# Optimization experiments

Measured on AMD Instinct MI355X. Metric: run time of the kernel, lower is better.

The kernel has to match this reference:

```python
import jax, jax.numpy as jnp
import numpy as np

N = 500_000
MOL_C = 128
HID_C = 256
NUM_GRAPHS = 16384


def setup_inputs() -> dict:
    key = jax.random.key(0)
    ks = jax.random.split(key, 7)
    fan_lin = (MOL_C + HID_C) ** -0.5
    fan_last = HID_C ** -0.5
    return {
        "input_rep": jax.random.normal(ks[0], (N, MOL_C), dtype=jnp.float32),
        "final_rep": jax.random.normal(ks[1], (N, HID_C), dtype=jnp.float32),
        "graph_index": jnp.sort(jax.random.randint(ks[2], (N,), 0, NUM_GRAPHS, dtype=jnp.int32)),
        "W_lin": jax.random.normal(ks[3], (HID_C, MOL_C + HID_C), dtype=jnp.float32) * fan_lin,
        "b_lin": jax.random.normal(ks[4], (HID_C,), dtype=jnp.float32) * fan_lin,
        "W_last": jax.random.normal(ks[5], (HID_C, HID_C), dtype=jnp.float32) * fan_last,
        "b_last": jax.random.normal(ks[6], (HID_C,), dtype=jnp.float32) * fan_last,
    }


def reference(input_rep, final_rep, graph_index, W_lin, b_lin, W_last, b_last):
    # att = sigmoid(Linear(cat([input_rep, final_rep], dim=1)))  -> [N, HID_C]
    cat = jnp.concatenate([input_rep, final_rep], axis=1)
    att = jax.nn.sigmoid(cat @ W_lin.T + b_lin)
    # gated value: att * Linear(final_rep)  -> [N, HID_C]
    g = att * (final_rep @ W_last.T + b_last)
    # scatter_add over nodes -> [NUM_GRAPHS, HID_C]
    return jax.ops.segment_sum(g, graph_index, num_segments=NUM_GRAPHS)
```

## Files before the change

### kernel.cpp

```cpp
#include <hip/hip_runtime.h>
#include <hip/hip_bf16.h>

#define MOLC 128
#define HIDC 256
#define KTOT 384
#define TILE_N 128
#define NTHREADS 512
#define APAD 40
#define WPAD 40

typedef _Float16 f16;
typedef _Float16 f16x8 __attribute__((ext_vector_type(8)));
typedef float    f32x4 __attribute__((ext_vector_type(4)));

__device__ inline f16x8 cvt8(float4 a, float4 b) {
  f16x8 r;
  r[0] = (f16)a.x; r[1] = (f16)a.y; r[2] = (f16)a.z; r[3] = (f16)a.w;
  r[4] = (f16)b.x; r[5] = (f16)b.y; r[6] = (f16)b.z; r[7] = (f16)b.w;
  return r;
}

__global__ void zero_out_kernel(float4* __restrict__ p, int n4) {
  int i = blockIdx.x * blockDim.x + threadIdx.x;
  if (i < n4) p[i] = make_float4(0.f, 0.f, 0.f, 0.f);
}

__global__ __launch_bounds__(NTHREADS, 2) void attn_pool_kernel(
    const float* __restrict__ input_rep,
    const float* __restrict__ final_rep,
    const int*   __restrict__ gidx,
    const float* __restrict__ W_lin,
    const float* __restrict__ b_lin,
    const float* __restrict__ W_last,
    const float* __restrict__ b_last,
    float* __restrict__ out,
    int n_nodes)
{
  __shared__ f16 A_lds[TILE_N * APAD];
  __shared__ f16 W1_lds[HIDC * WPAD];
  __shared__ f16 W2_lds[HIDC * WPAD];
  __shared__ int gi_lds[TILE_N];

  const int t    = threadIdx.x;
  const int nb   = blockIdx.x * TILE_N;
  const int vn   = min(TILE_N, n_nodes - nb);

  const int lane = t & 63;
  const int w    = t >> 6;
  const int h    = w >> 2;
  const int wch  = (w & 3) * 64;
  const int lr   = lane & 15;
  const int lq   = lane >> 4;

  if (t < TILE_N) gi_lds[t] = (nb + t < n_nodes) ? gidx[nb + t] : -1;

  f32x4 acc1[4][4];
  f32x4 acc2[4][4];
#pragma unroll
  for (int i = 0; i < 4; ++i)
#pragma unroll
    for (int j = 0; j < 4; ++j) {
      acc1[i][j] = (f32x4)(0.f);
      acc2[i][j] = (f32x4)(0.f);
    }

  const int arow = t >> 2;
  const int acol = (t & 3) * 8;
  const int wrow = t >> 1;
  const int wcol = (t & 1) * 16;

  for (int ks = 0; ks < 12; ++ks) {
    const int k0 = ks * 32;

    {
      float4 x0, x1;
      if (arow < vn) {
        const float* src = (ks < 4)
            ? (input_rep + (size_t)(nb + arow) * MOLC + (k0 + acol))
            : (final_rep + (size_t)(nb + arow) * HIDC + (k0 - MOLC + acol));
        x0 = *(const float4*)src;
        x1 = *(const float4*)(src + 4);
      } else {
        x0 = make_float4(0.f, 0.f, 0.f, 0.f);
        x1 = x0;
      }
      *(f16x8*)&A_lds[arow * APAD + acol] = cvt8(x0, x1);
    }

    {
      const float* src = W_lin + (size_t)wrow * KTOT + (k0 + wcol);
      float4 a = ((const float4*)src)[0];
      float4 b = ((const float4*)src)[1];
      float4 c = ((const float4*)src)[2];
      float4 d = ((const float4*)src)[3];
      *(f16x8*)&W1_lds[wrow * WPAD + wcol]     = cvt8(a, b);
      *(f16x8*)&W1_lds[wrow * WPAD + wcol + 8] = cvt8(c, d);
    }

    if (ks >= 4) {
      const float* src = W_last + (size_t)wrow * HIDC + (k0 - MOLC + wcol);
      float4 a = ((const float4*)src)[0];
      float4 b = ((const float4*)src)[1];
      float4 c = ((const float4*)src)[2];
      float4 d = ((const float4*)src)[3];
      *(f16x8*)&W2_lds[wrow * WPAD + wcol]     = cvt8(a, b);
      *(f16x8*)&W2_lds[wrow * WPAD + wcol + 8] = cvt8(c, d);
    }

    __syncthreads();

    f16x8 af[4];
#pragma unroll
    for (int i = 0; i < 4; ++i)
      af[i] = *(const f16x8*)&A_lds[(h * 64 + i * 16 + lr) * APAD + lq * 8];

    {
      f16x8 bf[4];
#pragma unroll
      for (int j = 0; j < 4; ++j)
        bf[j] = *(const f16x8*)&W1_lds[(wch + j * 16 + lr) * WPAD + lq * 8];
#pragma unroll
      for (int i = 0; i < 4; ++i)
#pragma unroll
        for (int j = 0; j < 4; ++j)
          acc1[i][j] = __builtin_amdgcn_mfma_f32_16x16x32_f16(af[i], bf[j], acc1[i][j], 0, 0, 0);
    }
    if (ks >= 4) {
      f16x8 bf[4];
#pragma unroll
      for (int j = 0; j < 4; ++j)
        bf[j] = *(const f16x8*)&W2_lds[(wch + j * 16 + lr) * WPAD + lq * 8];
#pragma unroll
      for (int i = 0; i < 4; ++i)
#pragma unroll
        for (int j = 0; j < 4; ++j)
          acc2[i][j] = __builtin_amdgcn_mfma_f32_16x16x32_f16(af[i], bf[j], acc2[i][j], 0, 0, 0);
    }

    __syncthreads();
  }

  float bl[4], bb[4];
#pragma unroll
  for (int j = 0; j < 4; ++j) {
    bl[j] = b_lin[wch + j * 16 + lr];
    bb[j] = b_last[wch + j * 16 + lr];
  }
#pragma unroll
  for (int i = 0; i < 4; ++i)
#pragma unroll
    for (int j = 0; j < 4; ++j)
#pragma unroll
      for (int r = 0; r < 4; ++r) {
        float a   = acc1[i][j][r] + bl[j];
        float att = 1.f / (1.f + __expf(-a));
        acc1[i][j][r] = att * (acc2[i][j][r] + bb[j]);
      }

  for (int i = 0; i < 4; ++i) {
    const int base = h * 64 + i * 16;
    int myg[4];
#pragma unroll
    for (int r = 0; r < 4; ++r) myg[r] = gi_lds[base + lq * 4 + r];

    int s = 0;
    while (s < 16) {
      const int gid = gi_lds[base + s];
      int e = s + 1;
      while (e < 16 && gi_lds[base + e] == gid) ++e;
      if (gid >= 0) {
#pragma unroll
        for (int j = 0; j < 4; ++j) {
          float v = 0.f;
#pragma unroll
          for (int r = 0; r < 4; ++r)
            if (myg[r] == gid) v += acc1[i][j][r];
          v += __shfl_xor(v, 16);
          v += __shfl_xor(v, 32);
          if (lane < 16)
            atomicAdd(&out[(size_t)gid * HIDC + wch + j * 16 + lane], v);
        }
      }
      s = e;
    }
  }
}

extern "C" void kernel_launch(void* const* d_in, const int* in_sizes, int n_in,
                              void* d_out, int out_size, void* d_ws, size_t ws_size,
                              hipStream_t stream) {
  const float* input_rep = (const float*)d_in[0];
  const float* final_rep = (const float*)d_in[1];
  const int*   gidx      = (const int*)d_in[2];
  const float* W_lin     = (const float*)d_in[3];
  const float* b_lin     = (const float*)d_in[4];
  const float* W_last    = (const float*)d_in[5];
  const float* b_last    = (const float*)d_in[6];
  float* out = (float*)d_out;

  const int n_nodes = in_sizes[0] / MOLC;

  const int n4 = out_size / 4;
  zero_out_kernel<<<(n4 + 255) / 256, 256, 0, stream>>>((float4*)out, n4);

  const int grid = (n_nodes + TILE_N - 1) / TILE_N;
  attn_pool_kernel<<<grid, NTHREADS, 0, stream>>>(
      input_rep, final_rep, gidx, W_lin, b_lin, W_last, b_last, out, n_nodes);
}
```

Before: 1.242 ms.

## Prepack fp16 swizzled weights and double-buffer tiles with async LDS loads

Adds a pre-pass that converts W_lin and W_last to fp16 in a tile-major, XOR-swizzled layout in the workspace. The main kernel then stages weight tiles directly into LDS with global_load_lds and double-buffers weights and activations so the next K-slice loads overlap the MFMA work. The tile shrinks to 64 nodes with 256 threads, and the swizzle replaces LDS padding to avoid bank conflicts. This removes per-block fp32-to-fp16 weight conversion, but each block now re-reads the weights for half as many nodes, and one extra kernel launch is added.

```diff
diff --git a/kernel.cpp b/kernel.cpp
--- a/kernel.cpp
+++ b/kernel.cpp
@@ -1,124 +1,151 @@
 #include <hip/hip_runtime.h>
 #include <hip/hip_bf16.h>
+
 
 #define MOLC 128
 #define HIDC 256
 #define KTOT 384
-#define TILE_N 128
-#define NTHREADS 512
-#define APAD 40
-#define WPAD 40
+#define NKT  12
+#define TILE_N 64
+#define NTHREADS 256
 
 typedef _Float16 f16;
 typedef _Float16 f16x8 __attribute__((ext_vector_type(8)));
 typedef float    f32x4 __attribute__((ext_vector_type(4)));
 
-__device__ inline f16x8 cvt8(float4 a, float4 b) {
+__device__ __host__ __forceinline__ int swz(int r) { return (r ^ (r >> 2)) & 3; }
+
+__device__ __forceinline__ f16x8 cvt8(float4 a, float4 b) {
   f16x8 r;
   r[0] = (f16)a.x; r[1] = (f16)a.y; r[2] = (f16)a.z; r[3] = (f16)a.w;
   r[4] = (f16)b.x; r[5] = (f16)b.y; r[6] = (f16)b.z; r[7] = (f16)b.w;
   return r;
 }
 
+#define GLL16(g, l) __builtin_amdgcn_global_load_lds(                          \
+    (const __attribute__((address_space(1))) uint32_t*)(g),                    \
+    (__attribute__((address_space(3))) uint32_t*)(l), 16, 0, 0)
+
 __global__ void zero_out_kernel(float4* __restrict__ p, int n4) {
   int i = blockIdx.x * blockDim.x + threadIdx.x;
   if (i < n4) p[i] = make_float4(0.f, 0.f, 0.f, 0.f);
+}
+
+__global__ void pack_weights_kernel(const float* __restrict__ W_lin,
+                                    const float* __restrict__ W_last,
+                                    f16* __restrict__ ws) {
+  int s = blockIdx.x * blockDim.x + threadIdx.x;
+  if (s >= 20480) return;
+  const float* src;
+  f16* dst;
+  if (s < 12288) {
+    int ks = s >> 10, r = (s >> 2) & 255, c = s & 3;
+    src = W_lin + (size_t)r * KTOT + ks * 32 + ((c ^ swz(r)) * 8);
+    dst = ws + (size_t)s * 8;
+  } else {
+    int s2 = s - 12288;
+    int ks = s2 >> 10, r = (s2 >> 2) & 255, c = s2 & 3;
+    src = W_last + (size_t)r * HIDC + ks * 32 + ((c ^ swz(r)) * 8);
+    dst = ws + 98304 + (size_t)s2 * 8;
+  }
+  f16x8 v;
+#pragma unroll
+  for (int j = 0; j < 8; ++j) v[j] = (f16)src[j];
+  *(f16x8*)dst = v;
+}
+
+__device__ __forceinline__ void stage_w(const f16* gtile, f16* ltile, int wv, int lane) {
+#pragma unroll
+  for (int c = 0; c < 4; ++c) {
+    const int off = (wv * 4 + c) * 1024 + lane * 16;
+    GLL16((const char*)gtile + off, (char*)ltile + off);
+  }
 }
 
 __global__ __launch_bounds__(NTHREADS, 2) void attn_pool_kernel(
     const float* __restrict__ input_rep,
     const float* __restrict__ final_rep,
     const int*   __restrict__ gidx,
-    const float* __restrict__ W_lin,
+    const f16*   __restrict__ ws,
     const float* __restrict__ b_lin,
-    const float* __restrict__ W_last,
     const float* __restrict__ b_last,
     float* __restrict__ out,
     int n_nodes)
 {
-  __shared__ f16 A_lds[TILE_N * APAD];
-  __shared__ f16 W1_lds[HIDC * WPAD];
-  __shared__ f16 W2_lds[HIDC * WPAD];
-  __shared__ int gi_lds[TILE_N];
+  __shared__ f16 Abuf[2][TILE_N * 32];
+  __shared__ f16 W1buf[2][HIDC * 32];
+  __shared__ f16 W2buf[2][HIDC * 32];
+  __shared__ int gi[TILE_N];
 
   const int t    = threadIdx.x;
   const int nb   = blockIdx.x * TILE_N;
   const int vn   = min(TILE_N, n_nodes - nb);
-
   const int lane = t & 63;
-  const int w    = t >> 6;
-  const int h    = w >> 2;
-  const int wch  = (w & 3) * 64;
+  const int wv   = t >> 6;
+  const int wch  = wv * 64;
   const int lr   = lane & 15;
   const int lq   = lane >> 4;
-
-  if (t < TILE_N) gi_lds[t] = (nb + t < n_nodes) ? gidx[nb + t] : -1;
-
-  f32x4 acc1[4][4];
-  f32x4 acc2[4][4];
+  const int sl   = (lq ^ swz(lr)) * 8;
+
+  const int arow  = t >> 2;
+  const int aslot = t & 3;
+  const int awslot = (aslot ^ swz(arow)) * 8;
+
+  if (t < TILE_N) gi[t] = (nb + t < n_nodes) ? gidx[nb + t] : -1;
+
+  const f16* wsW1 = ws;
+  const f16* wsW2 = ws + 98304;
+
+  stage_w(wsW1, W1buf[0], wv, lane);
+  {
+    float4 x0, x1;
+    if (arow < vn) {
+      const float* src = input_rep + (size_t)(nb + arow) * MOLC + aslot * 8;
+      x0 = ((const float4*)src)[0];
+      x1 = ((const float4*)src)[1];
+    } else {
+      x0 = make_float4(0.f, 0.f, 0.f, 0.f); x1 = x0;
+    }
+    *(f16x8*)&Abuf[0][arow * 32 + awslot] = cvt8(x0, x1);
+  }
+  __syncthreads();
+
+  f32x4 acc1[4][4], acc2[4][4];
 #pragma unroll
   for (int i = 0; i < 4; ++i)
 #pragma unroll
-    for (int j = 0; j < 4; ++j) {
-      acc1[i][j] = (f32x4)(0.f);
-      acc2[i][j] = (f32x4)(0.f);
-    }
-
-  const int arow = t >> 2;
-  const int acol = (t & 3) * 8;
-  const int wrow = t >> 1;
-  const int wcol = (t & 1) * 16;
-
-  for (int ks = 0; ks < 12; ++ks) {
-    const int k0 = ks * 32;
-
-    {
-      float4 x0, x1;
+    for (int j = 0; j < 4; ++j) { acc1[i][j] = (f32x4)(0.f); acc2[i][j] = (f32x4)(0.f); }
+
+  for (int ks = 0; ks < NKT; ++ks) {
+    const int cur = ks & 1, nxt = cur ^ 1;
+    const int kn  = ks + 1;
+    const bool pf = (kn < NKT);
+
+    float4 x0, x1;
+    if (pf) {
+      stage_w(wsW1 + kn * 8192, W1buf[nxt], wv, lane);
+      if (kn >= 4) stage_w(wsW2 + (kn - 4) * 8192, W2buf[nxt], wv, lane);
       if (arow < vn) {
-        const float* src = (ks < 4)
-            ? (input_rep + (size_t)(nb + arow) * MOLC + (k0 + acol))
-            : (final_rep + (size_t)(nb + arow) * HIDC + (k0 - MOLC + acol));
-        x0 = *(const float4*)src;
-        x1 = *(const float4*)(src + 4);
+        const float* src = (kn < 4)
+            ? input_rep + (size_t)(nb + arow) * MOLC + kn * 32 + aslot * 8
+            : final_rep + (size_t)(nb + arow) * HIDC + (kn * 32 - MOLC) + aslot * 8;
+        x0 = ((const float4*)src)[0];
+        x1 = ((const float4*)src)[1];
       } else {
-        x0 = make_float4(0.f, 0.f, 0.f, 0.f);
-        x1 = x0;
+        x0 = make_float4(0.f, 0.f, 0.f, 0.f); x1 = x0;
       }
-      *(f16x8*)&A_lds[arow * APAD + acol] = cvt8(x0, x1);
-    }
-
-    {
-      const float* src = W_lin + (size_t)wrow * KTOT + (k0 + wcol);
-      float4 a = ((const float4*)src)[0];
-      float4 b = ((const float4*)src)[1];
-      float4 c = ((const float4*)src)[2];
-      float4 d = ((const float4*)src)[3];
-      *(f16x8*)&W1_lds[wrow * WPAD + wcol]     = cvt8(a, b);
-      *(f16x8*)&W1_lds[wrow * WPAD + wcol + 8] = cvt8(c, d);
-    }
-
-    if (ks >= 4) {
-      const float* src = W_last + (size_t)wrow * HIDC + (k0 - MOLC + wcol);
-      float4 a = ((const float4*)src)[0];
-      float4 b = ((const float4*)src)[1];
-      float4 c = ((const float4*)src)[2];
-      float4 d = ((const float4*)src)[3];
-      *(f16x8*)&W2_lds[wrow * WPAD + wcol]     = cvt8(a, b);
-      *(f16x8*)&W2_lds[wrow * WPAD + wcol + 8] = cvt8(c, d);
-    }
-
-    __syncthreads();
+    }
 
     f16x8 af[4];
 #pragma unroll
     for (int i = 0; i < 4; ++i)
-      af[i] = *(const f16x8*)&A_lds[(h * 64 + i * 16 + lr) * APAD + lq * 8];
+      af[i] = *(const f16x8*)&Abuf[cur][(i * 16 + lr) * 32 + sl];
 
     {
       f16x8 bf[4];
 #pragma unroll
       for (int j = 0; j < 4; ++j)
-        bf[j] = *(const f16x8*)&W1_lds[(wch + j * 16 + lr) * WPAD + lq * 8];
+        bf[j] = *(const f16x8*)&W1buf[cur][(wch + j * 16 + lr) * 32 + sl];
 #pragma unroll
       for (int i = 0; i < 4; ++i)
 #pragma unroll
@@ -129,13 +156,15 @@
       f16x8 bf[4];
 #pragma unroll
       for (int j = 0; j < 4; ++j)
-        bf[j] = *(const f16x8*)&W2_lds[(wch + j * 16 + lr) * WPAD + lq * 8];
+        bf[j] = *(const f16x8*)&W2buf[cur][(wch + j * 16 + lr) * 32 + sl];
 #pragma unroll
       for (int i = 0; i < 4; ++i)
 #pragma unroll
         for (int j = 0; j < 4; ++j)
           acc2[i][j] = __builtin_amdgcn_mfma_f32_16x16x32_f16(af[i], bf[j], acc2[i][j], 0, 0, 0);
     }
+
+    if (pf) *(f16x8*)&Abuf[nxt][arow * 32 + awslot] = cvt8(x0, x1);
 
     __syncthreads();
   }
@@ -158,16 +187,16 @@
       }
 
   for (int i = 0; i < 4; ++i) {
-    const int base = h * 64 + i * 16;
+    const int base = i * 16;
     int myg[4];
 #pragma unroll
-    for (int r = 0; r < 4; ++r) myg[r] = gi_lds[base + lq * 4 + r];
+    for (int r = 0; r < 4; ++r) myg[r] = gi[base + lq * 4 + r];
 
     int s = 0;
     while (s < 16) {
-      const int gid = gi_lds[base + s];
+      const int gid = gi[base + s];
       int e = s + 1;
-      while (e < 16 && gi_lds[base + e] == gid) ++e;
+      while (e < 16 && gi[base + e] == gid) ++e;
       if (gid >= 0) {
 #pragma unroll
         for (int j = 0; j < 4; ++j) {
@@ -197,13 +226,16 @@
   const float* W_last    = (const float*)d_in[5];
   const float* b_last    = (const float*)d_in[6];
   float* out = (float*)d_out;
+  f16*   ws  = (f16*)d_ws;
 
   const int n_nodes = in_sizes[0] / MOLC;
 
   const int n4 = out_size / 4;
   zero_out_kernel<<<(n4 + 255) / 256, 256, 0, stream>>>((float4*)out, n4);
 
+  pack_weights_kernel<<<80, 256, 0, stream>>>(W_lin, W_last, ws);
+
   const int grid = (n_nodes + TILE_N - 1) / TILE_N;
   attn_pool_kernel<<<grid, NTHREADS, 0, stream>>>(
-      input_rep, final_rep, gidx, W_lin, b_lin, W_last, b_last, out, n_nodes);
-}
+      input_rep, final_rep, gidx, ws, b_lin, b_last, out, n_nodes);
+}
```

Result: faster. 1.022 ms (-17.7%).
